# Kernel optimization log

Hardware: AMD Instinct MI355X
Metric: run time of the kernel (lower is better)

The kernel has to match this reference:

```python
import jax, jax.numpy as jnp
import numpy as np

N, C, K = 4096, 10000, 64

def setup_inputs() -> dict:
    key = jax.random.key(0)
    k1, k2, k3 = jax.random.split(key, 3)
    input = jax.random.normal(k1, (N, C), dtype=jnp.float32)
    target = jax.random.randint(k2, (N,), 0, C, dtype=jnp.int64)
    dont_care = jax.random.randint(k3, (N, K), 0, C, dtype=jnp.int64)
    return {"input": input, "target": target, "dont_care": dont_care}

def reference(input, target, dont_care):
    n, c = input.shape
    # dc_mask[n, j] = True iff class j appears in dont_care[n]
    rows = jnp.arange(n)[:, None]  # [N,1]
    dc_mask = jnp.zeros((n, c), dtype=bool).at[rows, dont_care].set(True)
    is_target = jnp.arange(c)[None, :] == target[:, None]  # [N,C]
    # target branch takes precedence over dont_care (matches original if/elif)
    per_elem = jnp.where(is_target, (1.0 - input) ** 2,
                         jnp.where(dc_mask, 0.0, input ** 2))
    return jnp.sum(per_elem)
```

## Files before the change

kernel.cpp:

```cpp
#include <hip/hip_runtime.h>

#define N_ROWS 4096
#define N_COLS 10000
#define K_DC   64
#define NTHR   256
#define RPB    2
#define NBLK   (N_ROWS / RPB)
#define ELEMS  (RPB * N_COLS)
#define VECS   (ELEMS / 4)
#define MASK_WORDS (ELEMS / 32)

__global__ __launch_bounds__(NTHR) void dcl_partial(
    const float* __restrict__ input,
    const int* __restrict__ target,
    const int* __restrict__ dont_care,
    float* __restrict__ partials)
{
    const int b   = blockIdx.x;
    const int tid = threadIdx.x;

    __shared__ unsigned mask[MASK_WORDS];
    __shared__ int trow[RPB];

    for (int w = tid; w < MASK_WORDS; w += NTHR) mask[w] = 0u;
    if (tid < RPB) trow[tid] = target[b * RPB + tid];
    __syncthreads();

    if (tid < RPB * K_DC) {
        const int w = tid >> 6;
        const int k = tid & 63;
        const int c = dont_care[(b * RPB + w) * K_DC + k];
        const int bitpos = w * N_COLS + c;
        atomicOr(&mask[bitpos >> 5], 1u << (bitpos & 31));
    } else if (tid < RPB * K_DC + RPB) {
        const int w = tid - RPB * K_DC;
        const int bitpos = w * N_COLS + trow[w];
        atomicOr(&mask[bitpos >> 5], 1u << (bitpos & 31));
    }
    __syncthreads();

    float a0 = 0.f, a1 = 0.f, a2 = 0.f, a3 = 0.f;
    const float4* __restrict__ chunk =
        (const float4*)input + (long long)b * VECS;

#define PROC(I, ACC)                                                          \
    {                                                                         \
        const int ii = (I);                                                   \
        float4 v = chunk[ii];                                                 \
        ACC += v.x * v.x + v.y * v.y + v.z * v.z + v.w * v.w;                 \
        unsigned nib = (mask[ii >> 3] >> ((ii & 7) * 4)) & 0xFu;              \
        if (nib) {                                                            \
            float e[4] = { v.x, v.y, v.z, v.w };                              \
            _Pragma("unroll")                                                 \
            for (int j = 0; j < 4; ++j) {                                     \
                if (nib & (1u << j)) {                                        \
                    const int cic = 4 * ii + j;             \
                    const int r   = (cic >= N_COLS) ? 1 : 0;                  \
                    const int c   = cic - r * N_COLS;                         \
                    const float x = e[j];                                     \
                    if (c == trow[r])                                         \
                        ACC += (1.f - x) * (1.f - x) - x * x;     \
                    else                                                      \
                        ACC -= x * x;                     \
                }                                                             \
            }                                                                 \
        }                                                                     \
    }

    int i = tid;
    for (; i + 3 * NTHR < VECS; i += 4 * NTHR) {
        PROC(i,            a0)
        PROC(i + NTHR,     a1)
        PROC(i + 2 * NTHR, a2)
        PROC(i + 3 * NTHR, a3)
    }
    for (; i < VECS; i += NTHR)
        PROC(i, a0)
#undef PROC

    float acc = (a0 + a1) + (a2 + a3);

    const int lane = tid & 63;
    #pragma unroll
    for (int off = 32; off > 0; off >>= 1)
        acc += __shfl_down(acc, off, 64);

    __shared__ float warp_sums[NTHR / 64];
    if (lane == 0) warp_sums[tid >> 6] = acc;
    __syncthreads();
    if (tid == 0) {
        partials[b] = (warp_sums[0] + warp_sums[1]) +
                      (warp_sums[2] + warp_sums[3]);
    }
}

__global__ __launch_bounds__(NTHR) void dcl_reduce(
    const float* __restrict__ partials,
    float* __restrict__ out)
{
    const float4* __restrict__ p4 = (const float4*)partials;
    float s = 0.f;
    #pragma unroll
    for (int i = threadIdx.x; i < NBLK / 4; i += NTHR) {
        float4 v = p4[i];
        s += (v.x + v.y) + (v.z + v.w);
    }
    #pragma unroll
    for (int off = 32; off > 0; off >>= 1)
        s += __shfl_down(s, off, 64);
    __shared__ float warp_sums[NTHR / 64];
    const int lane = threadIdx.x & 63;
    if (lane == 0) warp_sums[threadIdx.x >> 6] = s;
    __syncthreads();
    if (threadIdx.x == 0)
        out[0] = (warp_sums[0] + warp_sums[1]) + (warp_sums[2] + warp_sums[3]);
}

extern "C" void kernel_launch(void* const* d_in, const int* in_sizes, int n_in,
                              void* d_out, int out_size, void* d_ws, size_t ws_size,
                              hipStream_t stream)
{
    const float* input     = (const float*)d_in[0];
    const int*   target    = (const int*)d_in[1];
    const int*   dont_care = (const int*)d_in[2];
    float* out      = (float*)d_out;
    float* partials = (float*)d_ws;

    dcl_partial<<<NBLK, NTHR, 0, stream>>>(input, target, dont_care, partials);
    dcl_reduce<<<1, NTHR, 0, stream>>>(partials, out);
}
```

Baseline: 31.75 us.

## Overlap dense sum-of-squares stream with mask build, apply corrections via sparse bit scan

The kernel now starts streaming the input and accumulating x^2 right away, while the don't-care indices load and the shared mask is zeroed. It no longer waits on the barrier and mask build before the main loop. Corrections are then applied in a separate pass that walks the set bits of the mask and re-reads only the flagged elements, which are likely still in cache. This takes the per-vector LDS mask lookup and branch out of the hot loop, at the cost of a second, sparse global read and a divergent bit-scan loop.

```diff
diff --git a/kernel.cpp b/kernel.cpp
--- a/kernel.cpp
+++ b/kernel.cpp
@@ -22,15 +22,40 @@
     __shared__ unsigned mask[MASK_WORDS];
     __shared__ int trow[RPB];
 
-    for (int w = tid; w < MASK_WORDS; w += NTHR) mask[w] = 0u;
-    if (tid < RPB) trow[tid] = target[b * RPB + tid];
+    int dc_c = 0;
+    if (tid < RPB * K_DC)
+        dc_c = dont_care[(b * RPB + (tid >> 6)) * K_DC + (tid & 63)];
+    if (tid < RPB)
+        trow[tid] = target[b * RPB + tid];
+    for (int w = tid; w < MASK_WORDS; w += NTHR)
+        mask[w] = 0u;
+
+    float a0 = 0.f, a1 = 0.f, a2 = 0.f, a3 = 0.f;
+    const float4* __restrict__ chunk =
+        (const float4*)input + (long long)b * VECS;
+
+    int i = tid;
+    for (; i + 3 * NTHR < VECS; i += 4 * NTHR) {
+        float4 v0 = chunk[i];
+        float4 v1 = chunk[i +     NTHR];
+        float4 v2 = chunk[i + 2 * NTHR];
+        float4 v3 = chunk[i + 3 * NTHR];
+        a0 += v0.x * v0.x + v0.y * v0.y + v0.z * v0.z + v0.w * v0.w;
+        a1 += v1.x * v1.x + v1.y * v1.y + v1.z * v1.z + v1.w * v1.w;
+        a2 += v2.x * v2.x + v2.y * v2.y + v2.z * v2.z + v2.w * v2.w;
+        a3 += v3.x * v3.x + v3.y * v3.y + v3.z * v3.z + v3.w * v3.w;
+    }
+    for (; i < VECS; i += NTHR) {
+        float4 v = chunk[i];
+        a0 += v.x * v.x + v.y * v.y + v.z * v.z + v.w * v.w;
+    }
+
+    float acc = (a0 + a1) + (a2 + a3);
+
     __syncthreads();
-
     if (tid < RPB * K_DC) {
         const int w = tid >> 6;
-        const int k = tid & 63;
-        const int c = dont_care[(b * RPB + w) * K_DC + k];
-        const int bitpos = w * N_COLS + c;
+        const int bitpos = w * N_COLS + dc_c;
         atomicOr(&mask[bitpos >> 5], 1u << (bitpos & 31));
     } else if (tid < RPB * K_DC + RPB) {
         const int w = tid - RPB * K_DC;
@@ -39,46 +64,22 @@
     }
     __syncthreads();
 
-    float a0 = 0.f, a1 = 0.f, a2 = 0.f, a3 = 0.f;
-    const float4* __restrict__ chunk =
-        (const float4*)input + (long long)b * VECS;
-
-#define PROC(I, ACC)                                                          \
-    {                                                                         \
-        const int ii = (I);                                                   \
-        float4 v = chunk[ii];                                                 \
-        ACC += v.x * v.x + v.y * v.y + v.z * v.z + v.w * v.w;                 \
-        unsigned nib = (mask[ii >> 3] >> ((ii & 7) * 4)) & 0xFu;              \
-        if (nib) {                                                            \
-            float e[4] = { v.x, v.y, v.z, v.w };                              \
-            _Pragma("unroll")                                                 \
-            for (int j = 0; j < 4; ++j) {                                     \
-                if (nib & (1u << j)) {                                        \
-                    const int cic = 4 * ii + j;             \
-                    const int r   = (cic >= N_COLS) ? 1 : 0;                  \
-                    const int c   = cic - r * N_COLS;                         \
-                    const float x = e[j];                                     \
-                    if (c == trow[r])                                         \
-                        ACC += (1.f - x) * (1.f - x) - x * x;     \
-                    else                                                      \
-                        ACC -= x * x;                     \
-                }                                                             \
-            }                                                                 \
-        }                                                                     \
+    const float* __restrict__ base = input + (long long)b * ELEMS;
+    for (int w = tid; w < MASK_WORDS; w += NTHR) {
+        unsigned m = mask[w];
+        while (m) {
+            const int bit = __ffs(m) - 1;
+            m &= m - 1;
+            const int bitpos = w * 32 + bit;
+            const int r = (bitpos >= N_COLS) ? 1 : 0;
+            const int c = bitpos - r * N_COLS;
+            const float x = base[bitpos];
+            if (c == trow[r])
+                acc += (1.f - x) * (1.f - x) - x * x;
+            else
+                acc -= x * x;
+        }
     }
-
-    int i = tid;
-    for (; i + 3 * NTHR < VECS; i += 4 * NTHR) {
-        PROC(i,            a0)
-        PROC(i + NTHR,     a1)
-        PROC(i + 2 * NTHR, a2)
-        PROC(i + 3 * NTHR, a3)
-    }
-    for (; i < VECS; i += NTHR)
-        PROC(i, a0)
-#undef PROC
-
-    float acc = (a0 + a1) + (a2 + a3);
 
     const int lane = tid & 63;
     #pragma unroll
```

Result: slower. 35.06 us (+10.4%).

## Fuse final reduction into main kernel via last-block counter and nontemporal loads

Applied to the files above, without the earlier changes.

Merges the partial-sum kernel and the single-block reduce kernel into one launch. The last block to finish, detected with an atomic counter after a threadfence, sums all partials. Input loads become nontemporal vector loads to avoid polluting cache with streamed data. A hipMemsetAsync is added each call to reset the counter, which replaces one kernel launch with a memset node and adds atomic and fence overhead.

```diff
diff --git a/kernel.cpp b/kernel.cpp
--- a/kernel.cpp
+++ b/kernel.cpp
@@ -10,17 +10,23 @@
 #define VECS   (ELEMS / 4)
 #define MASK_WORDS (ELEMS / 32)
 
-__global__ __launch_bounds__(NTHR) void dcl_partial(
+typedef float f32x4 __attribute__((ext_vector_type(4)));
+
+__global__ __launch_bounds__(NTHR) void dcl_fused(
     const float* __restrict__ input,
     const int* __restrict__ target,
     const int* __restrict__ dont_care,
-    float* __restrict__ partials)
+    float* __restrict__ partials,
+    unsigned* __restrict__ counter,
+    float* __restrict__ out)
 {
     const int b   = blockIdx.x;
     const int tid = threadIdx.x;
 
     __shared__ unsigned mask[MASK_WORDS];
     __shared__ int trow[RPB];
+    __shared__ float warp_sums[NTHR / 64];
+    __shared__ bool is_last;
 
     for (int w = tid; w < MASK_WORDS; w += NTHR) mask[w] = 0u;
     if (tid < RPB) trow[tid] = target[b * RPB + tid];
@@ -40,24 +46,23 @@
     __syncthreads();
 
     float a0 = 0.f, a1 = 0.f, a2 = 0.f, a3 = 0.f;
-    const float4* __restrict__ chunk =
-        (const float4*)input + (long long)b * VECS;
+    const f32x4* __restrict__ chunk =
+        (const f32x4*)input + (long long)b * VECS;
 
 #define PROC(I, ACC)                                                          \
     {                                                                         \
         const int ii = (I);                                                   \
-        float4 v = chunk[ii];                                                 \
-        ACC += v.x * v.x + v.y * v.y + v.z * v.z + v.w * v.w;                 \
+        f32x4 v = __builtin_nontemporal_load(&chunk[ii]);                     \
+        ACC += v[0] * v[0] + v[1] * v[1] + v[2] * v[2] + v[3] * v[3];         \
         unsigned nib = (mask[ii >> 3] >> ((ii & 7) * 4)) & 0xFu;              \
         if (nib) {                                                            \
-            float e[4] = { v.x, v.y, v.z, v.w };                              \
             _Pragma("unroll")                                                 \
             for (int j = 0; j < 4; ++j) {                                     \
                 if (nib & (1u << j)) {                                        \
                     const int cic = 4 * ii + j;             \
                     const int r   = (cic >= N_COLS) ? 1 : 0;                  \
                     const int c   = cic - r * N_COLS;                         \
-                    const float x = e[j];                                     \
+                    const float x = v[j];                                     \
                     if (c == trow[r])                                         \
                         ACC += (1.f - x) * (1.f - x) - x * x;     \
                     else                                                      \
@@ -85,35 +90,35 @@
     for (int off = 32; off > 0; off >>= 1)
         acc += __shfl_down(acc, off, 64);
 
-    __shared__ float warp_sums[NTHR / 64];
     if (lane == 0) warp_sums[tid >> 6] = acc;
     __syncthreads();
+
     if (tid == 0) {
-        partials[b] = (warp_sums[0] + warp_sums[1]) +
-                      (warp_sums[2] + warp_sums[3]);
+        const float bsum = (warp_sums[0] + warp_sums[1]) +
+                           (warp_sums[2] + warp_sums[3]);
+        partials[b] = bsum;
+        __threadfence();
+        const unsigned prev = atomicAdd(counter, 1u);
+        is_last = (prev == NBLK - 1);
     }
-}
+    __syncthreads();
 
-__global__ __launch_bounds__(NTHR) void dcl_reduce(
-    const float* __restrict__ partials,
-    float* __restrict__ out)
-{
-    const float4* __restrict__ p4 = (const float4*)partials;
-    float s = 0.f;
-    #pragma unroll
-    for (int i = threadIdx.x; i < NBLK / 4; i += NTHR) {
-        float4 v = p4[i];
-        s += (v.x + v.y) + (v.z + v.w);
+    if (is_last) {
+        __threadfence();
+        float s = 0.f;
+        #pragma unroll
+        for (int i2 = tid; i2 < NBLK; i2 += NTHR)
+            s += __hip_atomic_load(&partials[i2], __ATOMIC_RELAXED,
+                                   __HIP_MEMORY_SCOPE_AGENT);
+        #pragma unroll
+        for (int off = 32; off > 0; off >>= 1)
+            s += __shfl_down(s, off, 64);
+        if (lane == 0) warp_sums[tid >> 6] = s;
+        __syncthreads();
+        if (tid == 0)
+            out[0] = (warp_sums[0] + warp_sums[1]) +
+                     (warp_sums[2] + warp_sums[3]);
     }
-    #pragma unroll
-    for (int off = 32; off > 0; off >>= 1)
-        s += __shfl_down(s, off, 64);
-    __shared__ float warp_sums[NTHR / 64];
-    const int lane = threadIdx.x & 63;
-    if (lane == 0) warp_sums[threadIdx.x >> 6] = s;
-    __syncthreads();
-    if (threadIdx.x == 0)
-        out[0] = (warp_sums[0] + warp_sums[1]) + (warp_sums[2] + warp_sums[3]);
 }
 
 extern "C" void kernel_launch(void* const* d_in, const int* in_sizes, int n_in,
@@ -124,8 +129,10 @@
     const int*   target    = (const int*)d_in[1];
     const int*   dont_care = (const int*)d_in[2];
     float* out      = (float*)d_out;
-    float* partials = (float*)d_ws;
+    float*    partials = (float*)d_ws;
+    unsigned* counter  = (unsigned*)((char*)d_ws + NBLK * sizeof(float));
 
-    dcl_partial<<<NBLK, NTHR, 0, stream>>>(input, target, dont_care, partials);
-    dcl_reduce<<<1, NTHR, 0, stream>>>(partials, out);
+    hipMemsetAsync(counter, 0, sizeof(unsigned), stream);
+    dcl_fused<<<NBLK, NTHR, 0, stream>>>(input, target, dont_care,
+                                         partials, counter, out);
 }
```

After: 91.04 us. 187% more time.
